# Kernel optimization log

Measured on AMD Instinct MI355X. Metric: run time of the kernel, lower is better.

## Reference

```python
import jax, jax.numpy as jnp
import numpy as np

N = 8192
IN_DIM = 512
HID = 512


def setup_inputs() -> dict:
    key = jax.random.key(0)
    k1, k2, k3, k4 = jax.random.split(key, 4)
    input_features = jax.random.normal(k1, (N, IN_DIM), dtype=jnp.float32)
    # positive weighted adjacency so degrees > 0
    adjacency_matrix = jax.random.uniform(k2, (N, N), dtype=jnp.float32)
    # xavier_init: normal with std = 1/sqrt(in_dim/2)
    Wgcn1 = jax.random.normal(k3, (IN_DIM, HID), dtype=jnp.float32) * (1.0 / np.sqrt(IN_DIM / 2.0))
    bgcn1 = jnp.zeros((HID,), dtype=jnp.float32)
    Wgcn12 = jax.random.normal(k4, (HID, HID), dtype=jnp.float32) * (1.0 / np.sqrt(HID / 2.0))
    bgcn12 = jnp.zeros((HID,), dtype=jnp.float32)
    return {
        "input_features": input_features,
        "adjacency_matrix": adjacency_matrix,
        "Wgcn1": Wgcn1,
        "bgcn1": bgcn1,
        "Wgcn12": Wgcn12,
        "bgcn12": bgcn12,
    }


def reference(input_features, adjacency_matrix, Wgcn1, bgcn1, Wgcn12, bgcn12):
    # D^{-1/2} A D^{-1/2}: diag matmuls expressed as row/col elementwise scaling
    # (mathematically identical to torch.matmul(diag(d), A @ diag(d)))
    d_inv_sqrt = jnp.power(adjacency_matrix.sum(axis=1), -0.5)  # [N]
    norm_adj = d_inv_sqrt[:, None] * adjacency_matrix * d_inv_sqrt[None, :]  # [N, N]

    support = input_features @ Wgcn1            # [N, HID]
    out = norm_adj @ support + bgcn1            # [N, HID]
    out = jax.nn.relu(out)                      # dropout p=0.0 -> identity
    support = out @ Wgcn12                      # [N, HID]
    out = norm_adj @ support + bgcn12           # [N, HID]
    return out
```

## Files before the change

### kernel.cpp

```cpp
#include <hip/hip_runtime.h>
#include <stdint.h>


typedef __attribute__((ext_vector_type(8))) __bf16 bf16x8;
typedef __attribute__((ext_vector_type(4))) float f32x4;
typedef __attribute__((ext_vector_type(8))) unsigned short u16x8;

__device__ __forceinline__ unsigned short f2bf(float f) {
  union { float f; uint32_t u; } v; v.f = f;
  uint32_t u = v.u;
  return (unsigned short)((u + 0x7fffu + ((u >> 16) & 1u)) >> 16);
}

__device__ __forceinline__ float bf2f(unsigned short u) {
  union { uint32_t u; float f; } v; v.u = ((uint32_t)u) << 16; return v.f;
}

__device__ __forceinline__ void async_cp16(const void* g, void* lds) {
  auto gp = (const __attribute__((address_space(1))) uint32_t*)g;
  auto lp = (__attribute__((address_space(3))) uint32_t*)lds;
  __builtin_amdgcn_global_load_lds(gp, lp, 16, 0, 0);
}

__global__ __launch_bounds__(256) void k_rowsum_convert(
    const float* __restrict__ A, unsigned short* __restrict__ Abf,
    float* __restrict__ dvec, int ncols) {
  const int row = blockIdx.x;
  const float* arow = A + (size_t)row * ncols;
  unsigned short* orow = Abf + (size_t)row * ncols;
  float s = 0.f;
  for (int c = threadIdx.x * 4; c < ncols; c += 256 * 4) {
    float4 v = *(const float4*)(arow + c);
    s += (v.x + v.y) + (v.z + v.w);
    ushort4 o;
    o.x = f2bf(v.x); o.y = f2bf(v.y); o.z = f2bf(v.z); o.w = f2bf(v.w);
    *(ushort4*)(orow + c) = o;
  }
  #pragma unroll
  for (int off = 32; off > 0; off >>= 1) s += __shfl_down(s, off);
  __shared__ float red[4];
  if ((threadIdx.x & 63) == 0) red[threadIdx.x >> 6] = s;
  __syncthreads();
  if (threadIdx.x == 0) {
    float t = (red[0] + red[1]) + (red[2] + red[3]);
    dvec[row] = 1.0f / sqrtf(t);
  }
}

__global__ __launch_bounds__(256) void k_f32_to_bf16(
    const float* __restrict__ in, unsigned short* __restrict__ out, int n4) {
  int i = blockIdx.x * 256 + threadIdx.x;
  if (i < n4) {
    float4 v = ((const float4*)in)[i];
    ushort4 o;
    o.x = f2bf(v.x); o.y = f2bf(v.y); o.z = f2bf(v.z); o.w = f2bf(v.w);
    ((ushort4*)out)[i] = o;
  }
}

__global__ __launch_bounds__(256) void k_transpose_bf16(
    const float* __restrict__ in, unsigned short* __restrict__ out, int dim) {
  int o = blockIdx.x * 256 + threadIdx.x;
  if (o < dim * dim) {
    int k = o % dim;
    int n = o / dim;
    out[o] = f2bf(in[k * dim + n]);
  }
}

template <int MODE>
__global__ __launch_bounds__(256, 2) void gemm_bt(
    const unsigned short* __restrict__ Aop,
    const unsigned short* __restrict__ Bt,
    void* __restrict__ Cout,
    const float* __restrict__ dvec,
    const float* __restrict__ bias,
    int M, int N, int K) {
  constexpr int BM = 128, BN = 64, BK = 32;
  __shared__ unsigned short As[BM * BK];
  __shared__ unsigned short Bs[BN * BK];

  const int tid = threadIdx.x;
  const int w = tid >> 6;
  const int l = tid & 63;
  const int rowBase = blockIdx.y * BM;
  const int colBase = blockIdx.x * BN;
  const int waveM = w >> 1;
  const int waveN = w & 1;

  f32x4 acc[4][2];
  const f32x4 fz = {0.f, 0.f, 0.f, 0.f};
  #pragma unroll
  for (int m = 0; m < 4; ++m)
    #pragma unroll
    for (int n = 0; n < 2; ++n) acc[m][n] = fz;

  const int chunkRow = l >> 2;
  const int kOff = (l & 3) * 8;
  const unsigned short* gA0 = Aop + (size_t)(rowBase + w * 16 + chunkRow) * K + kOff;
  const unsigned short* gA1 = gA0 + (size_t)64 * K;
  const unsigned short* gB0 = Bt + (size_t)(colBase + w * 16 + chunkRow) * K + kOff;
  unsigned short* lA0 = As + w * 512;
  unsigned short* lA1 = As + (w + 4) * 512;
  unsigned short* lB0 = Bs + w * 512;

  const int kfrag = (l >> 4) * 8;
  const int lrow = l & 15;

  for (int k0 = 0; k0 < K; k0 += BK) {
    async_cp16(gA0 + k0, lA0);
    async_cp16(gA1 + k0, lA1);
    async_cp16(gB0 + k0, lB0);
    __syncthreads();

    bf16x8 af[4], bfr[2];
    #pragma unroll
    for (int m = 0; m < 4; ++m)
      af[m] = *(const bf16x8*)(As + (waveM * 64 + m * 16 + lrow) * BK + kfrag);
    #pragma unroll
    for (int n = 0; n < 2; ++n)
      bfr[n] = *(const bf16x8*)(Bs + (waveN * 32 + n * 16 + lrow) * BK + kfrag);

    #pragma unroll
    for (int m = 0; m < 4; ++m)
      #pragma unroll
      for (int n = 0; n < 2; ++n)
        acc[m][n] = __builtin_amdgcn_mfma_f32_16x16x32_bf16(af[m], bfr[n],
                                                            acc[m][n], 0, 0, 0);
    __syncthreads();
  }

  const int erow0 = rowBase + waveM * 64 + (l >> 4) * 4;
  const int ecol0 = colBase + waveN * 32 + (l & 15);
  #pragma unroll
  for (int m = 0; m < 4; ++m) {
    #pragma unroll
    for (int n = 0; n < 2; ++n) {
      #pragma unroll
      for (int j = 0; j < 4; ++j) {
        const int rowg = erow0 + m * 16 + j;
        const int colg = ecol0 + n * 16;
        float v = acc[m][n][j];
        if (MODE == 0) {
          v *= dvec[colg];
          ((unsigned short*)Cout)[(size_t)rowg * N + colg] = f2bf(v);
        }
      }
    }
  }
}

__global__ __launch_bounds__(512, 1) void gemm_big3f(
    const unsigned short* __restrict__ Aop,
    const unsigned short* __restrict__ Bt,
    unsigned short* __restrict__ Pout,
    int M, int N, int K, int kLen) {
  constexpr int BK = 32;
  __shared__ char lds[3 * 32768];

  const int tid = threadIdx.x;
  const int w = tid >> 6;
  const int l = tid & 63;

  const int id = blockIdx.x;
  const int q = id & 7, s = id >> 3;
  const int bx = s & 1;
  const int by = ((q & 1) << 4) | (s >> 1);
  const int bz = q >> 1;

  const int rowBase = by * 256;
  const int colBase = bx * 256;
  const int kBase = bz * kLen;
  const int waveM = w >> 2;
  const int waveN = w & 3;

  f32x4 acc[8][4];
  const f32x4 fz = {0.f, 0.f, 0.f, 0.f};
  #pragma unroll
  for (int m = 0; m < 8; ++m)
    #pragma unroll
    for (int n = 0; n < 4; ++n) acc[m][n] = fz;

  const int srcElem = ((l & 3) ^ ((l >> 3) & 3)) * 8;
  const unsigned short* aSrc =
      Aop + (size_t)(rowBase + w * 32 + (l >> 2)) * K + kBase + srcElem;
  const unsigned short* bSrc =
      Bt + (size_t)(colBase + w * 32 + (l >> 2)) * K + kBase + srcElem;
  const int dstTh = w * 2048 + l * 16;

#define STAGE_A(tt, bb)                                                   \
  {                                                                       \
    const size_t o = (size_t)(tt) * BK;                                   \
    async_cp16(aSrc + o, lds + (bb) + dstTh);                             \
    async_cp16(aSrc + (size_t)16 * K + o, lds + (bb) + dstTh + 1024);     \
  }
#define STAGE_B(tt, bb)                                                   \
  {                                                                       \
    const size_t o = (size_t)(tt) * BK;                                   \
    async_cp16(bSrc + o, lds + (bb) + 16384 + dstTh);                     \
    async_cp16(bSrc + (size_t)16 * K + o, lds + (bb) + 16384 + dstTh + 1024); \
  }

  const int nt = kLen / BK;
  STAGE_A(0, 0); STAGE_B(0, 0);
  STAGE_A(1, 32768); STAGE_B(1, 32768);

  const int lrow = l & 15;
  const int kq = l >> 4;
  const int xr = (lrow >> 1) & 3;
  const int slotByte = ((kq ^ xr) << 4);
  const int aRow0 = (waveM * 128 + lrow) * 64;
  const int bRow0 = 16384 + (waveN * 64 + lrow) * 64;

  int cur = 0, nxt = 32768, fut = 65536;
  for (int t = 0; t < nt; ++t) {
    if (t == nt - 1) {
      asm volatile("s_waitcnt vmcnt(0)" ::: "memory");
    } else {
      asm volatile("s_waitcnt vmcnt(4)" ::: "memory");
    }
    __builtin_amdgcn_s_barrier();

    bf16x8 af[4], bfr[4], af2[4];
    #pragma unroll
    for (int i = 0; i < 4; ++i)
      af[i] = *(const bf16x8*)(lds + cur + aRow0 + i * 16 * 64 + slotByte);
    #pragma unroll
    for (int n = 0; n < 4; ++n)
      bfr[n] = *(const bf16x8*)(lds + cur + bRow0 + n * 16 * 64 + slotByte);
    if (t + 2 < nt) STAGE_A(t + 2, fut);

    #pragma unroll
    for (int i = 0; i < 4; ++i)
      #pragma unroll
      for (int n = 0; n < 4; ++n)
        acc[i][n] = __builtin_amdgcn_mfma_f32_16x16x32_bf16(
            af[i], bfr[n], acc[i][n], 0, 0, 0);

    #pragma unroll
    for (int i = 0; i < 4; ++i)
      af2[i] = *(const bf16x8*)(lds + cur + aRow0 + (64 + i * 16) * 64 + slotByte);
    if (t + 2 < nt) STAGE_B(t + 2, fut);

    #pragma unroll
    for (int i = 0; i < 4; ++i)
      #pragma unroll
      for (int n = 0; n < 4; ++n)
        acc[4 + i][n] = __builtin_amdgcn_mfma_f32_16x16x32_bf16(
            af2[i], bfr[n], acc[4 + i][n], 0, 0, 0);

    const int tmp = cur; cur = nxt; nxt = fut; fut = tmp;
  }
#undef STAGE_A
#undef STAGE_B

  unsigned short* pz = Pout + (size_t)bz * M * N;
  const int erow0 = rowBase + waveM * 128 + (l >> 4) * 4;
  const int ecol0 = colBase + waveN * 64 + (l & 15);
  #pragma unroll
  for (int m = 0; m < 8; ++m) {
    #pragma unroll
    for (int n = 0; n < 4; ++n) {
      #pragma unroll
      for (int j = 0; j < 4; ++j) {
        pz[(size_t)(erow0 + m * 16 + j) * N + ecol0 + n * 16] =
            f2bf(acc[m][n][j]);
      }
    }
  }
}

template <int MODE>
__global__ __launch_bounds__(256) void k_reduce(
    const unsigned short* __restrict__ parts,
    const float* __restrict__ dvec,
    const float* __restrict__ bias,
    void* __restrict__ outp, int M, int N) {
  const size_t MN = (size_t)M * N;
  const size_t idx = ((size_t)blockIdx.x * 256 + threadIdx.x) * 8;
  if (idx >= MN) return;
  const int row = (int)(idx / N);
  const int col = (int)(idx % N);
  const float di = dvec[row];
  float s[8] = {0, 0, 0, 0, 0, 0, 0, 0};
  #pragma unroll
  for (int z = 0; z < 4; ++z) {
    u16x8 v = *(const u16x8*)(parts + z * MN + idx);
    #pragma unroll
    for (int e = 0; e < 8; ++e) s[e] += bf2f(v[e]);
  }
  if (MODE == 1) {
    ushort4 o0, o1;
    unsigned short tmp[8];
    #pragma unroll
    for (int e = 0; e < 8; ++e) {
      float v = di * s[e] + bias[col + e];
      v = v > 0.f ? v : 0.f;
      tmp[e] = f2bf(v);
    }
    o0.x = tmp[0]; o0.y = tmp[1]; o0.z = tmp[2]; o0.w = tmp[3];
    o1.x = tmp[4]; o1.y = tmp[5]; o1.z = tmp[6]; o1.w = tmp[7];
    *(ushort4*)((unsigned short*)outp + idx) = o0;
    *(ushort4*)((unsigned short*)outp + idx + 4) = o1;
  } else {
    float4 o0, o1;
    o0.x = di * s[0] + bias[col + 0];
    o0.y = di * s[1] + bias[col + 1];
    o0.z = di * s[2] + bias[col + 2];
    o0.w = di * s[3] + bias[col + 3];
    o1.x = di * s[4] + bias[col + 4];
    o1.y = di * s[5] + bias[col + 5];
    o1.z = di * s[6] + bias[col + 6];
    o1.w = di * s[7] + bias[col + 7];
    *(float4*)((float*)outp + idx) = o0;
    *(float4*)((float*)outp + idx + 4) = o1;
  }
}

extern "C" void kernel_launch(void* const* d_in, const int* in_sizes, int n_in,
                              void* d_out, int out_size, void* d_ws, size_t ws_size,
                              hipStream_t stream) {
  const float* X  = (const float*)d_in[0];
  const float* A  = (const float*)d_in[1];
  const float* W1 = (const float*)d_in[2];
  const float* b1 = (const float*)d_in[3];
  const float* W2 = (const float*)d_in[4];
  const float* b2 = (const float*)d_in[5];
  float* out = (float*)d_out;

  constexpr int NN = 8192, IN = 512, HID = 512;
  constexpr int KSPLIT = 4;

  char* ws = (char*)d_ws;
  float* ddeg = (float*)ws;
  unsigned short* Abf = (unsigned short*)(ws + (32 << 10));
  unsigned short* W1t = Abf + (size_t)NN * NN;
  unsigned short* W2t = W1t + IN * HID;
  unsigned short* P0  = W2t + HID * HID;
  unsigned short* P1  = P0 + (size_t)NN * HID;
  unsigned short* parts = P1 + (size_t)NN * HID;

  k_rowsum_convert<<<NN, 256, 0, stream>>>(A, Abf, ddeg, NN);
  k_f32_to_bf16<<<(NN * IN / 4 + 255) / 256, 256, 0, stream>>>(X, P0, NN * IN / 4);
  k_transpose_bf16<<<(IN * HID + 255) / 256, 256, 0, stream>>>(W1, W1t, IN);
  k_transpose_bf16<<<(HID * HID + 255) / 256, 256, 0, stream>>>(W2, W2t, HID);

  gemm_bt<0><<<dim3(NN / 64, HID / 128), 256, 0, stream>>>(
      W1t, P0, P1, ddeg, nullptr, HID, NN, IN);
  gemm_big3f<<<2 * (NN / 256) * KSPLIT, 512, 0, stream>>>(
      Abf, P1, parts, NN, HID, NN, NN / KSPLIT);
  k_reduce<1><<<(int)((size_t)NN * HID / 8 / 256), 256, 0, stream>>>(
      parts, ddeg, b1, P0, NN, HID);
  gemm_bt<0><<<dim3(NN / 64, HID / 128), 256, 0, stream>>>(
      W2t, P0, P1, ddeg, nullptr, HID, NN, HID);
  gemm_big3f<<<2 * (NN / 256) * KSPLIT, 512, 0, stream>>>(
      Abf, P1, parts, NN, HID, NN, NN / KSPLIT);
  k_reduce<2><<<(int)((size_t)NN * HID / 8 / 256), 256, 0, stream>>>(
      parts, ddeg, b2, out, NN, HID);
}
```

Baseline: 259.7 us.

## Load B operand directly to registers and shrink LDS to double-buffered A

The big adjacency GEMM no longer stages the B operand through LDS. Each wave loads its B fragments straight from global memory into a register double buffer, while A keeps a two-stage LDS buffer instead of three. Launch bounds request two blocks per CU and MFMA sections get raised wave priority. This cuts LDS traffic and footprint, but adds duplicated global B reads across waves, a shallower pipeline with full waits each step, and register pressure under the tighter bound.

```diff
diff --git a/kernel.cpp b/kernel.cpp
--- a/kernel.cpp
+++ b/kernel.cpp
@@ -150,13 +150,13 @@
   }
 }
 
-__global__ __launch_bounds__(512, 1) void gemm_big3f(
+__global__ __launch_bounds__(512, 2) void gemm_bigRB(
     const unsigned short* __restrict__ Aop,
     const unsigned short* __restrict__ Bt,
     unsigned short* __restrict__ Pout,
     int M, int N, int K, int kLen) {
   constexpr int BK = 32;
-  __shared__ char lds[3 * 32768];
+  __shared__ char lds[2 * 16384];
 
   const int tid = threadIdx.x;
   const int w = tid >> 6;
@@ -184,8 +184,6 @@
   const int srcElem = ((l & 3) ^ ((l >> 3) & 3)) * 8;
   const unsigned short* aSrc =
       Aop + (size_t)(rowBase + w * 32 + (l >> 2)) * K + kBase + srcElem;
-  const unsigned short* bSrc =
-      Bt + (size_t)(colBase + w * 32 + (l >> 2)) * K + kBase + srcElem;
   const int dstTh = w * 2048 + l * 16;
 
 #define STAGE_A(tt, bb)                                                   \
@@ -194,65 +192,56 @@
     async_cp16(aSrc + o, lds + (bb) + dstTh);                             \
     async_cp16(aSrc + (size_t)16 * K + o, lds + (bb) + dstTh + 1024);     \
   }
-#define STAGE_B(tt, bb)                                                   \
-  {                                                                       \
-    const size_t o = (size_t)(tt) * BK;                                   \
-    async_cp16(bSrc + o, lds + (bb) + 16384 + dstTh);                     \
-    async_cp16(bSrc + (size_t)16 * K + o, lds + (bb) + 16384 + dstTh + 1024); \
-  }
-
-  const int nt = kLen / BK;
-  STAGE_A(0, 0); STAGE_B(0, 0);
-  STAGE_A(1, 32768); STAGE_B(1, 32768);
 
   const int lrow = l & 15;
   const int kq = l >> 4;
   const int xr = (lrow >> 1) & 3;
   const int slotByte = ((kq ^ xr) << 4);
   const int aRow0 = (waveM * 128 + lrow) * 64;
-  const int bRow0 = 16384 + (waveN * 64 + lrow) * 64;
-
-  int cur = 0, nxt = 32768, fut = 65536;
-  for (int t = 0; t < nt; ++t) {
-    if (t == nt - 1) {
-      asm volatile("s_waitcnt vmcnt(0)" ::: "memory");
-    } else {
-      asm volatile("s_waitcnt vmcnt(4)" ::: "memory");
-    }
-    __builtin_amdgcn_s_barrier();
-
-    bf16x8 af[4], bfr[4], af2[4];
-    #pragma unroll
-    for (int i = 0; i < 4; ++i)
-      af[i] = *(const bf16x8*)(lds + cur + aRow0 + i * 16 * 64 + slotByte);
-    #pragma unroll
-    for (int n = 0; n < 4; ++n)
-      bfr[n] = *(const bf16x8*)(lds + cur + bRow0 + n * 16 * 64 + slotByte);
-    if (t + 2 < nt) STAGE_A(t + 2, fut);
-
-    #pragma unroll
-    for (int i = 0; i < 4; ++i)
-      #pragma unroll
-      for (int n = 0; n < 4; ++n)
-        acc[i][n] = __builtin_amdgcn_mfma_f32_16x16x32_bf16(
-            af[i], bfr[n], acc[i][n], 0, 0, 0);
-
-    #pragma unroll
-    for (int i = 0; i < 4; ++i)
-      af2[i] = *(const bf16x8*)(lds + cur + aRow0 + (64 + i * 16) * 64 + slotByte);
-    if (t + 2 < nt) STAGE_B(t + 2, fut);
-
-    #pragma unroll
-    for (int i = 0; i < 4; ++i)
-      #pragma unroll
-      for (int n = 0; n < 4; ++n)
-        acc[4 + i][n] = __builtin_amdgcn_mfma_f32_16x16x32_bf16(
-            af2[i], bfr[n], acc[4 + i][n], 0, 0, 0);
-
-    const int tmp = cur; cur = nxt; nxt = fut; fut = tmp;
-  }
+
+  const unsigned short* bLane =
+      Bt + (size_t)(colBase + waveN * 64 + lrow) * K + kBase + kq * 8;
+
+  const int nt = kLen / BK;
+
+  STAGE_A(0, 0);
+  bf16x8 bA[4], bB[4];
+  #pragma unroll
+  for (int n = 0; n < 4; ++n)
+    bA[n] = *(const bf16x8*)(bLane + (size_t)n * 16 * K);
+
+#define BODY(t, bufoff, CUR, NXT)                                         \
+  {                                                                       \
+    asm volatile("s_waitcnt vmcnt(0)" ::: "memory");                      \
+    __builtin_amdgcn_s_barrier();                                         \
+    bf16x8 af[8];                                                         \
+    _Pragma("unroll")                                                     \
+    for (int i = 0; i < 8; ++i)                                           \
+      af[i] = *(const bf16x8*)(lds + (bufoff) + aRow0 + i * 16 * 64 +     \
+                               slotByte);                                 \
+    if ((t) + 1 < nt) {                                                   \
+      STAGE_A((t) + 1, (bufoff) ^ 16384);                                 \
+      _Pragma("unroll")                                                   \
+      for (int n = 0; n < 4; ++n)                                         \
+        NXT[n] = *(const bf16x8*)(bLane + (size_t)n * 16 * K +            \
+                                  (size_t)((t) + 1) * BK);                \
+    }                                                                     \
+    __builtin_amdgcn_s_setprio(1);                                        \
+    _Pragma("unroll")                                                     \
+    for (int i = 0; i < 8; ++i)                                           \
+      _Pragma("unroll")                                                   \
+      for (int n = 0; n < 4; ++n)                                         \
+        acc[i][n] = __builtin_amdgcn_mfma_f32_16x16x32_bf16(              \
+            af[i], CUR[n], acc[i][n], 0, 0, 0);                           \
+    __builtin_amdgcn_s_setprio(0);                                        \
+  }
+
+  for (int t2 = 0; t2 < nt; t2 += 2) {
+    BODY(t2, 0, bA, bB);
+    BODY(t2 + 1, 16384, bB, bA);
+  }
+#undef BODY
 #undef STAGE_A
-#undef STAGE_B
 
   unsigned short* pz = Pout + (size_t)bz * M * N;
   const int erow0 = rowBase + waveM * 128 + (l >> 4) * 4;
@@ -347,13 +336,13 @@
 
   gemm_bt<0><<<dim3(NN / 64, HID / 128), 256, 0, stream>>>(
       W1t, P0, P1, ddeg, nullptr, HID, NN, IN);
-  gemm_big3f<<<2 * (NN / 256) * KSPLIT, 512, 0, stream>>>(
+  gemm_bigRB<<<2 * (NN / 256) * KSPLIT, 512, 0, stream>>>(
       Abf, P1, parts, NN, HID, NN, NN / KSPLIT);
   k_reduce<1><<<(int)((size_t)NN * HID / 8 / 256), 256, 0, stream>>>(
       parts, ddeg, b1, P0, NN, HID);
   gemm_bt<0><<<dim3(NN / 64, HID / 128), 256, 0, stream>>>(
       W2t, P0, P1, ddeg, nullptr, HID, NN, HID);
-  gemm_big3f<<<2 * (NN / 256) * KSPLIT, 512, 0, stream>>>(
+  gemm_bigRB<<<2 * (NN / 256) * KSPLIT, 512, 0, stream>>>(
       Abf, P1, parts, NN, HID, NN, NN / KSPLIT);
   k_reduce<2><<<(int)((size_t)NN * HID / 8 / 256), 256, 0, stream>>>(
       parts, ddeg, b2, out, NN, HID);
```

After: 360.7 us. 38.9% more time.
